# Performance work log

Measured on AMD Instinct MI355X. Metric: run time of the kernel, lower is better.

The kernel has to match this reference:

```python
import jax, jax.numpy as jnp
import numpy as np

HIDDEN = 1024
HEADS = 16
HEAD_DIM = HIDDEN // HEADS
ROPE_BASE = 10000.0


def rope_cos_sin(seq_len, head_dim, dtype=jnp.float32):
    inv_freq = 1.0 / (ROPE_BASE ** (jnp.arange(0, head_dim, 2, dtype=jnp.float32) / head_dim))
    t = jnp.arange(seq_len, dtype=jnp.float32)
    freqs = jnp.einsum('i,j->ij', t, inv_freq)          # [L, head_dim/2]
    emb = jnp.concatenate([freqs, freqs], axis=-1)       # [L, head_dim]
    return emb.astype(dtype), jnp.cos(emb).astype(dtype), jnp.sin(emb).astype(dtype)


def rotate_half(x):
    half = x.shape[-1] // 2
    return jnp.concatenate([-x[..., half:], x[..., :half]], axis=-1)


def setup_inputs() -> dict:
    key = jax.random.key(0)
    kx, kq, kk, kv, ko = jax.random.split(key, 5)
    B, L = 4, 2048
    scale = 1.0 / np.sqrt(HIDDEN)
    x = jax.random.normal(kx, (B, L, HIDDEN), dtype=jnp.float32)
    Wq = jax.random.normal(kq, (HIDDEN, HIDDEN), dtype=jnp.float32) * scale
    Wk = jax.random.normal(kk, (HIDDEN, HIDDEN), dtype=jnp.float32) * scale
    Wv = jax.random.normal(kv, (HIDDEN, HIDDEN), dtype=jnp.float32) * scale
    Wo = jax.random.normal(ko, (HIDDEN, HIDDEN), dtype=jnp.float32) * scale
    return {"x": x, "Wq": Wq, "Wk": Wk, "Wv": Wv, "Wo": Wo}


def reference(x, Wq, Wk, Wv, Wo):
    B, L, D = x.shape
    H, Hd = HEADS, HEAD_DIM
    # projections (nn.Linear: y = x @ W.T; weights here stored already as [out,in])
    q = (x @ Wq.T).reshape(B, L, H, Hd).transpose(0, 2, 1, 3)  # [B,H,L,Hd]
    k = (x @ Wk.T).reshape(B, L, H, Hd).transpose(0, 2, 1, 3)
    v = (x @ Wv.T).reshape(B, L, H, Hd).transpose(0, 2, 1, 3)
    _, cos, sin = rope_cos_sin(L, Hd, x.dtype)                  # [L, Hd]
    cos = cos[None, None, :, :]
    sin = sin[None, None, :, :]
    q = q * cos + rotate_half(q) * sin
    k = k * cos + rotate_half(k) * sin
    scores = jnp.einsum('bhqd,bhkd->bhqk', q, k) / np.sqrt(Hd)  # [B,H,L,L]
    attn = jax.nn.softmax(scores, axis=-1)
    out = jnp.einsum('bhqk,bhkd->bhqd', attn, v)                # [B,H,L,Hd]
    out = out.transpose(0, 2, 1, 3).reshape(B, L, D)
    return out @ Wo.T
```

## Files before the change

kernel.cpp:

```cpp
#include <hip/hip_runtime.h>
#include <math.h>

#define BB 4
#define LL 2048
#define DD 1024
#define HH 16
#define HD 64
#define BL (BB*LL)

typedef __attribute__((ext_vector_type(8))) short bf16x8;
typedef __attribute__((ext_vector_type(4))) short bf16x4;
typedef __attribute__((ext_vector_type(4))) float f32x4;

__device__ inline short f2bf(float f) {
    union { float f; unsigned u; } v; v.f = f;
    unsigned r = v.u + 0x7fffu + ((v.u >> 16) & 1u);
    return (short)(r >> 16);
}

__device__ inline unsigned pk_bf16(float a, float b) {
    union { float f; unsigned u; } x, y; x.f = a; y.f = b;
    return (x.u >> 16) | (y.u & 0xffff0000u);
}

__device__ inline float exp2x(float x) {
#if __has_builtin(__builtin_amdgcn_exp2f)
    return __builtin_amdgcn_exp2f(x);
#else
    return exp2f(x);
#endif
}

__device__ inline f32x4 mfma16x16x16_bf16(bf16x4 a, bf16x4 b, f32x4 c) {
#if __has_builtin(__builtin_amdgcn_mfma_f32_16x16x16bf16_1k)
    return __builtin_amdgcn_mfma_f32_16x16x16bf16_1k(a, b, c, 0, 0, 0);
#elif __has_builtin(__builtin_amdgcn_mfma_f32_16x16x16_bf16)
    return __builtin_amdgcn_mfma_f32_16x16x16_bf16(a, b, c, 0, 0, 0);
#else
    f32x4 d;
    asm volatile("v_mfma_f32_16x16x16_bf16 %0, %1, %2, %3"
                 : "=v"(d) : "v"(a), "v"(b), "v"(c));
    return d;
#endif
}

__device__ inline void gload_lds16(const void* g, void* l) {
    __builtin_amdgcn_global_load_lds(
        (const __attribute__((address_space(1))) unsigned int*)g,
        (__attribute__((address_space(3))) unsigned int*)l, 16, 0, 0);
}

__global__ __launch_bounds__(256) void cast_kernel(
    const float* __restrict__ in, short* __restrict__ out, int n)
{
    int i = (blockIdx.x * 256 + threadIdx.x) * 8;
    float4 a = *(const float4*)(in + i);
    float4 b = *(const float4*)(in + i + 4);
    bf16x8 o;
    o[0]=f2bf(a.x); o[1]=f2bf(a.y); o[2]=f2bf(a.z); o[3]=f2bf(a.w);
    o[4]=f2bf(b.x); o[5]=f2bf(b.y); o[6]=f2bf(b.z); o[7]=f2bf(b.w);
    *(bf16x8*)(out + i) = o;
}

__global__ __launch_bounds__(256) void cast4_kernel(
    const float* __restrict__ w0, const float* __restrict__ w1,
    const float* __restrict__ w2, const float* __restrict__ w3,
    short* __restrict__ out)
{
    const int nw_blocks = (DD*DD) / 2048;
    int sel = blockIdx.x / nw_blocks;
    int blk = blockIdx.x % nw_blocks;
    const float* in = (sel == 0) ? w0 : (sel == 1) ? w1 : (sel == 2) ? w2 : w3;
    int i = (blk * 256 + threadIdx.x) * 8;
    float4 a = *(const float4*)(in + i);
    float4 b = *(const float4*)(in + i + 4);
    bf16x8 o;
    o[0]=f2bf(a.x); o[1]=f2bf(a.y); o[2]=f2bf(a.z); o[3]=f2bf(a.w);
    o[4]=f2bf(b.x); o[5]=f2bf(b.y); o[6]=f2bf(b.z); o[7]=f2bf(b.w);
    *(bf16x8*)(out + (size_t)sel * DD * DD + i) = o;
}

__global__ __launch_bounds__(256) void rope_tab_kernel(float2* __restrict__ tab)
{
    int idx = blockIdx.x * 256 + threadIdx.x;
    int lq = idx >> 5, f = idx & 31;
    float inv = __expf((float)f * (-9.210340371976184f / 32.0f));
    float s, c;
    sincosf((float)lq * inv, &s, &c);
    tab[idx] = make_float2(c, s);
}

__device__ inline void gemm_bt_128(const short* __restrict__ A,
                                   const short* __restrict__ B,
                                   short* Ash, short* Bsh,
                                   int i0, int n0, f32x4 (&acc)[4][4])
{
    const int t  = threadIdx.x;
    const int w  = t >> 6;
    const int l  = t & 63;
    const int g  = (t >> 4) & 3;
    const int ln = t & 15;
    const int rh = (w >> 1) * 64;
    const int ch = (w & 1) * 64;
    const int srow = w * 8 + (l >> 3);
    const int skol = (l & 7) * 8;

    for (int k0 = 0; k0 < DD; k0 += 64) {
        __syncthreads();
        const short* ga = A + (size_t)(i0 + srow) * DD + k0 + skol;
        const short* gb = B + (size_t)(n0 + srow) * DD + k0 + skol;
        short* la = Ash + w * 512;
        short* lb = Bsh + w * 512;
        #pragma unroll
        for (int j = 0; j < 4; ++j) {
            gload_lds16(ga + j * 32 * DD, la + j * 2048);
            gload_lds16(gb + j * 32 * DD, lb + j * 2048);
        }
        __syncthreads();

        #pragma unroll
        for (int kk = 0; kk < 2; ++kk) {
            bf16x8 af[4], bfr[4];
            #pragma unroll
            for (int mi = 0; mi < 4; ++mi)
                af[mi] = *(const bf16x8*)(Ash + (rh + mi*16 + ln)*64 + kk*32 + 8*g);
            #pragma unroll
            for (int nj = 0; nj < 4; ++nj)
                bfr[nj] = *(const bf16x8*)(Bsh + (ch + nj*16 + ln)*64 + kk*32 + 8*g);
            #pragma unroll
            for (int mi = 0; mi < 4; ++mi)
                #pragma unroll
                for (int nj = 0; nj < 4; ++nj)
                    acc[mi][nj] = __builtin_amdgcn_mfma_f32_16x16x32_bf16(
                        af[mi], bfr[nj], acc[mi][nj], 0, 0, 0);
        }
    }
}

__global__ __launch_bounds__(256) void qkv_mfma_kernel(
    const short* __restrict__ xb, const short* __restrict__ Wqb,
    const short* __restrict__ Wkb, const short* __restrict__ Wvb,
    const float2* __restrict__ rope_tab,
    short* __restrict__ Qo, short* __restrict__ Ko, short* __restrict__ Vo)
{
    __shared__ short Ash[128*64];
    __shared__ short Bsh[128*64];

    const int gid = blockIdx.x;
    const int r8  = gid & 7;
    const int u   = gid >> 3;
    const int i_idx = r8 * 8 + (u & 7);
    const int nz  = u >> 3;
    const int n_idx = nz & 7;
    const int z   = nz >> 3;

    const short* Wm = (z == 0) ? Wqb : ((z == 1) ? Wkb : Wvb);
    const int i0 = i_idx * 128;
    const int n0 = n_idx * 128;

    f32x4 acc[4][4];
    #pragma unroll
    for (int mi = 0; mi < 4; ++mi)
        #pragma unroll
        for (int nj = 0; nj < 4; ++nj) acc[mi][nj] = (f32x4){0.f,0.f,0.f,0.f};

    gemm_bt_128(xb, Wm, Ash, Bsh, i0, n0, acc);

    const int t  = threadIdx.x;
    const int w  = t >> 6;
    const int g  = (t >> 4) & 3;
    const int ln = t & 15;
    const int rh = (w >> 1) * 64;

    if (z == 2) {
        short* buf = Ash;
        const int b = i0 >> 11, l0 = i0 & (LL - 1);
        const int d = t >> 2;
        const int c = t & 3;
        #pragma unroll
        for (int hp = 0; hp < 2; ++hp) {
            __syncthreads();
            if ((w & 1) == hp) {
                #pragma unroll
                for (int nj = 0; nj < 4; ++nj)
                    #pragma unroll
                    for (int mi = 0; mi < 4; ++mi)
                        #pragma unroll
                        for (int r = 0; r < 4; ++r)
                            buf[(nj*16 + ln)*136 + rh + mi*16 + 4*g + r]
                                = f2bf(acc[mi][nj][r]);
            }
            __syncthreads();
            short* dst = Vo + ((size_t)((b*HH + n_idx*2 + hp)*HD + d)) * LL + l0;
            #pragma unroll
            for (int j = 0; j < 4; ++j)
                *(bf16x8*)(dst + c*8 + j*32) =
                    *(const bf16x8*)(buf + d*136 + c*8 + j*32);
        }
    } else {
        const int h = n_idx * 2 + (w & 1);
        short* Om = (z == 0) ? Qo : Ko;
        const float sc = (z == 0) ? 0.180336880111112f : 1.0f;
        #pragma unroll
        for (int mi = 0; mi < 4; ++mi)
            #pragma unroll
            for (int r = 0; r < 4; ++r) {
                int i = i0 + rh + mi*16 + 4*g + r;
                int b = i >> 11, lq = i & (LL - 1);
                float2 cs0 = rope_tab[lq*32 + ln];
                float2 cs1 = rope_tab[lq*32 + ln + 16];
                float r0 = (acc[mi][0][r]*cs0.x - acc[mi][2][r]*cs0.y) * sc;
                float r2 = (acc[mi][2][r]*cs0.x + acc[mi][0][r]*cs0.y) * sc;
                float r1 = (acc[mi][1][r]*cs1.x - acc[mi][3][r]*cs1.y) * sc;
                float r3 = (acc[mi][3][r]*cs1.x + acc[mi][1][r]*cs1.y) * sc;
                size_t base = ((size_t)(b*HH + h) * LL + lq) * HD;
                Om[base + ln     ] = f2bf(r0);
                Om[base + ln + 16] = f2bf(r1);
                Om[base + ln + 32] = f2bf(r2);
                Om[base + ln + 48] = f2bf(r3);
            }
    }
}

__global__ __launch_bounds__(256) void attn_kernel(
    const short* __restrict__ Q, const short* __restrict__ K,
    const short* __restrict__ VT, short* __restrict__ AO)
{
    __shared__ short Ksh[64*72];
    __shared__ short VTs[64*72];

    const int t  = threadIdx.x;
    const int w  = t >> 6;
    const int l  = t & 63;
    const int g  = l >> 4;
    const int ln = l & 15;

    const int bh = blockIdx.x;
    const int q0 = blockIdx.y * 128;
    const short* Qb  = Q  + ((size_t)bh * LL + q0 + w*32) * HD;
    const short* Kb  = K  + (size_t)bh * LL * HD;
    const short* VTb = VT + (size_t)bh * HD * LL;

    bf16x8 qb[2][2];
    #pragma unroll
    for (int qi = 0; qi < 2; ++qi) {
        qb[qi][0] = *(const bf16x8*)(Qb + (size_t)(qi*16 + ln)*HD + 8*g);
        qb[qi][1] = *(const bf16x8*)(Qb + (size_t)(qi*16 + ln)*HD + 32 + 8*g);
    }

    f32x4 O[2][4];
    #pragma unroll
    for (int qi = 0; qi < 2; ++qi)
        #pragma unroll
        for (int db = 0; db < 4; ++db) O[qi][db] = (f32x4){0.f,0.f,0.f,0.f};
    float l_acc[2] = {0.f, 0.f};

    const int sr = t >> 2;
    const int sc = (t & 3) << 4;

    for (int kt = 0; kt < LL; kt += 64) {
        bf16x8 k0 = *(const bf16x8*)(Kb  + (size_t)(kt + sr)*HD + sc);
        bf16x8 k1 = *(const bf16x8*)(Kb  + (size_t)(kt + sr)*HD + sc + 8);
        bf16x8 v0 = *(const bf16x8*)(VTb + (size_t)sr*LL + kt + sc);
        bf16x8 v1 = *(const bf16x8*)(VTb + (size_t)sr*LL + kt + sc + 8);
        __syncthreads();
        *(bf16x8*)(Ksh + sr*72 + sc)     = k0;
        *(bf16x8*)(Ksh + sr*72 + sc + 8) = k1;
        *(bf16x8*)(VTs + sr*72 + sc)     = v0;
        *(bf16x8*)(VTs + sr*72 + sc + 8) = v1;
        __syncthreads();

        uint2 pf[2][4];
        #pragma unroll
        for (int kb = 0; kb < 4; ++kb) {
            bf16x8 ka0 = *(const bf16x8*)(Ksh + (kb*16 + ln)*72 + 8*g);
            bf16x8 ka1 = *(const bf16x8*)(Ksh + (kb*16 + ln)*72 + 32 + 8*g);
            #pragma unroll
            for (int qi = 0; qi < 2; ++qi) {
                f32x4 S = (f32x4){0.f,0.f,0.f,0.f};
                S = __builtin_amdgcn_mfma_f32_16x16x32_bf16(ka0, qb[qi][0], S, 0, 0, 0);
                S = __builtin_amdgcn_mfma_f32_16x16x32_bf16(ka1, qb[qi][1], S, 0, 0, 0);
                float p0 = exp2x(S[0]), p1 = exp2x(S[1]);
                float p2 = exp2x(S[2]), p3 = exp2x(S[3]);
                l_acc[qi] += (p0 + p1) + (p2 + p3);
                pf[qi][kb].x = pk_bf16(p0, p1);
                pf[qi][kb].y = pk_bf16(p2, p3);
            }
        }

        #pragma unroll
        for (int kb = 0; kb < 4; ++kb) {
            bf16x4 pa0 = __builtin_bit_cast(bf16x4, pf[0][kb]);
            bf16x4 pa1 = __builtin_bit_cast(bf16x4, pf[1][kb]);
            #pragma unroll
            for (int db = 0; db < 4; ++db) {
                bf16x4 vf = *(const bf16x4*)(VTs + (db*16 + ln)*72 + kb*16 + 4*g);
                O[0][db] = mfma16x16x16_bf16(pa0, vf, O[0][db]);
                O[1][db] = mfma16x16x16_bf16(pa1, vf, O[1][db]);
            }
        }
    }

    const int b = bh >> 4, h = bh & 15;
    #pragma unroll
    for (int qi = 0; qi < 2; ++qi) {
        float lr = l_acc[qi];
        lr += __shfl_xor(lr, 16);
        lr += __shfl_xor(lr, 32);
        #pragma unroll
        for (int r = 0; r < 4; ++r) {
            float inv = 1.0f / __shfl(lr, 4*g + r);
            int q = q0 + w*32 + qi*16 + 4*g + r;
            size_t base = ((size_t)(b*LL + q)) * DD + h*HD;
            #pragma unroll
            for (int db = 0; db < 4; ++db)
                AO[base + db*16 + ln] = f2bf(O[qi][db][r] * inv);
        }
    }
}

__global__ __launch_bounds__(256) void oproj_mfma_kernel(
    const short* __restrict__ A, const short* __restrict__ Wob,
    float* __restrict__ out)
{
    __shared__ short Ash[128*64];
    __shared__ short Bsh[128*64];

    const int gid = blockIdx.x;
    const int r8  = gid & 7;
    const int u   = gid >> 3;
    const int i_idx = r8 * 8 + (u & 7);
    const int n_idx = u >> 3;
    const int i0 = i_idx * 128;
    const int n0 = n_idx * 128;

    f32x4 acc[4][4];
    #pragma unroll
    for (int mi = 0; mi < 4; ++mi)
        #pragma unroll
        for (int nj = 0; nj < 4; ++nj) acc[mi][nj] = (f32x4){0.f,0.f,0.f,0.f};

    gemm_bt_128(A, Wob, Ash, Bsh, i0, n0, acc);

    const int t  = threadIdx.x;
    const int w  = t >> 6;
    const int g  = (t >> 4) & 3;
    const int ln = t & 15;
    const int rh = (w >> 1) * 64;
    const int ch = (w & 1) * 64;

    #pragma unroll
    for (int mi = 0; mi < 4; ++mi)
        #pragma unroll
        for (int r = 0; r < 4; ++r) {
            size_t base = (size_t)(i0 + rh + mi*16 + 4*g + r) * DD + n0 + ch;
            #pragma unroll
            for (int nj = 0; nj < 4; ++nj)
                out[base + nj*16 + ln] = acc[mi][nj][r];
        }
}

extern "C" void kernel_launch(void* const* d_in, const int* in_sizes, int n_in,
                              void* d_out, int out_size, void* d_ws, size_t ws_size,
                              hipStream_t stream) {
    const float* x  = (const float*)d_in[0];
    const float* Wq = (const float*)d_in[1];
    const float* Wk = (const float*)d_in[2];
    const float* Wv = (const float*)d_in[3];
    const float* Wo = (const float*)d_in[4];
    float* out = (float*)d_out;

    const size_t n_x = (size_t)BL * DD;
    const size_t n_w = (size_t)DD * DD;
    short* xb  = (short*)d_ws;
    short* Wqb = xb  + n_x;
    short* Wkb = Wqb + n_w;
    short* Wvb = Wkb + n_w;
    short* Wob = Wvb + n_w;
    short* Q   = Wob + n_w;
    short* K   = Q   + n_x;
    short* VTg = K   + n_x;
    short* AOb = VTg + n_x;
    float2* tab = (float2*)(AOb + n_x);

    rope_tab_kernel<<<256, 256, 0, stream>>>(tab);
    cast_kernel<<<n_x/2048, 256, 0, stream>>>(x, xb, (int)n_x);
    cast4_kernel<<<4*(n_w/2048), 256, 0, stream>>>(Wq, Wk, Wv, Wo, Wqb);

    qkv_mfma_kernel<<<1536, 256, 0, stream>>>(xb, Wqb, Wkb, Wvb, tab, Q, K, VTg);

    dim3 g2(BB*HH, LL/128);
    attn_kernel<<<g2, 256, 0, stream>>>(Q, K, VTg, AOb);

    oproj_mfma_kernel<<<512, 256, 0, stream>>>(AOb, Wob, out);
}
```

Measured before the change: 291.2 us.

## Drop LDS staging in attention, read K/V fragments directly from global

The attention kernel no longer stages K and V^T tiles through shared memory with two barriers per tile. Each wave now reads its MFMA fragments straight from global memory (relying on L2/L1 for reuse) and handles 16 queries instead of 32, which doubles the grid. The PV MFMA operands are swapped so the output can be written as packed 4-wide stores. This removes the barriers and LDS traffic, but it also halves K/V reuse per loaded fragment and sends more uncoalesced global loads through the cache.

```diff
diff --git a/kernel.cpp b/kernel.cpp
--- a/kernel.cpp
+++ b/kernel.cpp
@@ -226,9 +226,6 @@
     const short* __restrict__ Q, const short* __restrict__ K,
     const short* __restrict__ VT, short* __restrict__ AO)
 {
-    __shared__ short Ksh[64*72];
-    __shared__ short VTs[64*72];
-
     const int t  = threadIdx.x;
     const int w  = t >> 6;
     const int l  = t & 63;
@@ -236,86 +233,66 @@
     const int ln = l & 15;
 
     const int bh = blockIdx.x;
-    const int q0 = blockIdx.y * 128;
-    const short* Qb  = Q  + ((size_t)bh * LL + q0 + w*32) * HD;
+    const int q0 = blockIdx.y * 64;
+    const short* Qb  = Q  + ((size_t)bh * LL + q0 + w*16) * HD;
     const short* Kb  = K  + (size_t)bh * LL * HD;
     const short* VTb = VT + (size_t)bh * HD * LL;
 
-    bf16x8 qb[2][2];
-    #pragma unroll
-    for (int qi = 0; qi < 2; ++qi) {
-        qb[qi][0] = *(const bf16x8*)(Qb + (size_t)(qi*16 + ln)*HD + 8*g);
-        qb[qi][1] = *(const bf16x8*)(Qb + (size_t)(qi*16 + ln)*HD + 32 + 8*g);
+    bf16x8 qb0 = *(const bf16x8*)(Qb + (size_t)ln*HD + 8*g);
+    bf16x8 qb1 = *(const bf16x8*)(Qb + (size_t)ln*HD + 32 + 8*g);
+
+    f32x4 O[4];
+    #pragma unroll
+    for (int db = 0; db < 4; ++db) O[db] = (f32x4){0.f,0.f,0.f,0.f};
+    float l_acc = 0.f;
+
+    const short* kfrag = Kb + (size_t)ln*HD + 8*g;
+    const short* vfrag = VTb + (size_t)ln*LL + 4*g;
+
+    for (int kt = 0; kt < LL; kt += 64) {
+        uint2 pf[4];
+        #pragma unroll
+        for (int kb = 0; kb < 4; ++kb) {
+            const short* kp = kfrag + (size_t)(kt + kb*16)*HD;
+            bf16x8 ka0 = *(const bf16x8*)(kp);
+            bf16x8 ka1 = *(const bf16x8*)(kp + 32);
+            f32x4 S = (f32x4){0.f,0.f,0.f,0.f};
+            S = __builtin_amdgcn_mfma_f32_16x16x32_bf16(ka0, qb0, S, 0, 0, 0);
+            S = __builtin_amdgcn_mfma_f32_16x16x32_bf16(ka1, qb1, S, 0, 0, 0);
+            float p0 = exp2x(S[0]), p1 = exp2x(S[1]);
+            float p2 = exp2x(S[2]), p3 = exp2x(S[3]);
+            l_acc += (p0 + p1) + (p2 + p3);
+            pf[kb].x = pk_bf16(p0, p1);
+            pf[kb].y = pk_bf16(p2, p3);
+        }
+
+        #pragma unroll
+        for (int kb = 0; kb < 4; ++kb) {
+            bf16x4 pb = __builtin_bit_cast(bf16x4, pf[kb]);
+            #pragma unroll
+            for (int db = 0; db < 4; ++db) {
+                bf16x4 vf = *(const bf16x4*)(vfrag + (size_t)(db*16)*LL + kt + kb*16);
+                O[db] = mfma16x16x16_bf16(vf, pb, O[db]);
+            }
+        }
     }
 
-    f32x4 O[2][4];
-    #pragma unroll
-    for (int qi = 0; qi < 2; ++qi)
-        #pragma unroll
-        for (int db = 0; db < 4; ++db) O[qi][db] = (f32x4){0.f,0.f,0.f,0.f};
-    float l_acc[2] = {0.f, 0.f};
-
-    const int sr = t >> 2;
-    const int sc = (t & 3) << 4;
-
-    for (int kt = 0; kt < LL; kt += 64) {
-        bf16x8 k0 = *(const bf16x8*)(Kb  + (size_t)(kt + sr)*HD + sc);
-        bf16x8 k1 = *(const bf16x8*)(Kb  + (size_t)(kt + sr)*HD + sc + 8);
-        bf16x8 v0 = *(const bf16x8*)(VTb + (size_t)sr*LL + kt + sc);
-        bf16x8 v1 = *(const bf16x8*)(VTb + (size_t)sr*LL + kt + sc + 8);
-        __syncthreads();
-        *(bf16x8*)(Ksh + sr*72 + sc)     = k0;
-        *(bf16x8*)(Ksh + sr*72 + sc + 8) = k1;
-        *(bf16x8*)(VTs + sr*72 + sc)     = v0;
-        *(bf16x8*)(VTs + sr*72 + sc + 8) = v1;
-        __syncthreads();
-
-        uint2 pf[2][4];
-        #pragma unroll
-        for (int kb = 0; kb < 4; ++kb) {
-            bf16x8 ka0 = *(const bf16x8*)(Ksh + (kb*16 + ln)*72 + 8*g);
-            bf16x8 ka1 = *(const bf16x8*)(Ksh + (kb*16 + ln)*72 + 32 + 8*g);
-            #pragma unroll
-            for (int qi = 0; qi < 2; ++qi) {
-                f32x4 S = (f32x4){0.f,0.f,0.f,0.f};
-                S = __builtin_amdgcn_mfma_f32_16x16x32_bf16(ka0, qb[qi][0], S, 0, 0, 0);
-                S = __builtin_amdgcn_mfma_f32_16x16x32_bf16(ka1, qb[qi][1], S, 0, 0, 0);
-                float p0 = exp2x(S[0]), p1 = exp2x(S[1]);
-                float p2 = exp2x(S[2]), p3 = exp2x(S[3]);
-                l_acc[qi] += (p0 + p1) + (p2 + p3);
-                pf[qi][kb].x = pk_bf16(p0, p1);
-                pf[qi][kb].y = pk_bf16(p2, p3);
-            }
-        }
-
-        #pragma unroll
-        for (int kb = 0; kb < 4; ++kb) {
-            bf16x4 pa0 = __builtin_bit_cast(bf16x4, pf[0][kb]);
-            bf16x4 pa1 = __builtin_bit_cast(bf16x4, pf[1][kb]);
-            #pragma unroll
-            for (int db = 0; db < 4; ++db) {
-                bf16x4 vf = *(const bf16x4*)(VTs + (db*16 + ln)*72 + kb*16 + 4*g);
-                O[0][db] = mfma16x16x16_bf16(pa0, vf, O[0][db]);
-                O[1][db] = mfma16x16x16_bf16(pa1, vf, O[1][db]);
-            }
-        }
-    }
+    float lr = l_acc;
+    lr += __shfl_xor(lr, 16);
+    lr += __shfl_xor(lr, 32);
+    float inv = 1.0f / lr;
 
     const int b = bh >> 4, h = bh & 15;
-    #pragma unroll
-    for (int qi = 0; qi < 2; ++qi) {
-        float lr = l_acc[qi];
-        lr += __shfl_xor(lr, 16);
-        lr += __shfl_xor(lr, 32);
-        #pragma unroll
-        for (int r = 0; r < 4; ++r) {
-            float inv = 1.0f / __shfl(lr, 4*g + r);
-            int q = q0 + w*32 + qi*16 + 4*g + r;
-            size_t base = ((size_t)(b*LL + q)) * DD + h*HD;
-            #pragma unroll
-            for (int db = 0; db < 4; ++db)
-                AO[base + db*16 + ln] = f2bf(O[qi][db][r] * inv);
-        }
+    const int q = q0 + w*16 + ln;
+    short* dst = AO + ((size_t)(b*LL + q)) * DD + h*HD + 4*g;
+    #pragma unroll
+    for (int db = 0; db < 4; ++db) {
+        bf16x4 o4;
+        o4[0] = f2bf(O[db][0] * inv);
+        o4[1] = f2bf(O[db][1] * inv);
+        o4[2] = f2bf(O[db][2] * inv);
+        o4[3] = f2bf(O[db][3] * inv);
+        *(bf16x4*)(dst + db*16) = o4;
     }
 }
 
@@ -389,7 +366,7 @@
 
     qkv_mfma_kernel<<<1536, 256, 0, stream>>>(xb, Wqb, Wkb, Wvb, tab, Q, K, VTg);
 
-    dim3 g2(BB*HH, LL/128);
+    dim3 g2(BB*HH, LL/64);
     attn_kernel<<<g2, 256, 0, stream>>>(Q, K, VTg, AOb);
 
     oproj_mfma_kernel<<<512, 256, 0, stream>>>(AOb, Wob, out);
```

Result: slower. 868.5 us (+198.2%).
